# Optimization experiments

Measured on AMD Instinct MI355X. Metric: run time of the kernel, lower is better.

## Reference

```python
import jax, jax.numpy as jnp
import numpy as np

N = 16384; C = 16; H = 256; W = 704
HEADS = 4; PTS = 4; K = 8; DH = C // HEADS
EPS = 1e-3  # BatchNorm eps from module

def _bn(x, g, b):
    # BatchNorm1d in training mode: batch statistics over N
    mu = x.mean(axis=0)
    var = x.var(axis=0)
    return (x - mu) * jax.lax.rsqrt(var + EPS) * g + b

def setup_inputs():
    key = jax.random.key(0)
    ks = jax.random.split(key, 20)
    def w(i, shape, s=0.25):
        return jax.random.normal(ks[i], shape, jnp.float32) * s
    grid_y = jax.random.randint(ks[0], (N,), 0, H)
    grid_x = jax.random.randint(ks[1], (N,), 0, W)
    return {
        "point_features": jax.random.normal(ks[2], (N, C), jnp.float32),
        "image_feat": jax.random.normal(ks[3], (C, H, W), jnp.float32),
        "image_grid": jnp.stack([grid_y, grid_x], axis=1),
        "Wk": w(4, (C, C)), "bk": w(5, (C,)), "gk": jnp.ones((C,)), "betak": jnp.zeros((C,)),
        "Wfc": w(6, (2, C)), "bfc": w(7, (C,)), "gfc": jnp.ones((C,)), "betafc": jnp.zeros((C,)),
        "Wt": w(8, (C, C)), "bt": w(9, (C,)), "gt": jnp.ones((C,)), "betat": jnp.zeros((C,)),
        "Woff": w(10, (C, HEADS * PTS * 2), 0.02), "boff": w(11, (HEADS * PTS * 2,), 0.5),
        "Wattn": w(12, (C, HEADS * PTS), 0.02), "battn": jnp.zeros((HEADS * PTS,)),
        "Wval": w(13, (C, C)), "bval": w(14, (C,)),
        "Wout": w(15, (C, C)), "bout": w(16, (C,)),
        "Wf": w(17, (2 * C, C)), "bf": w(18, (C,)), "gf": jnp.ones((C,)), "betaf": jnp.zeros((C,)),
    }

def _deform_attn(q, image_feat, grid_f, Woff, boff, Wattn, battn, Wval, bval, Wout, bout):
    # MSDeformAttn with 1 level: learned offsets around projected pixel, bilinear sampling
    n = q.shape[0]
    off = (q @ Woff + boff).reshape(n, HEADS, PTS, 2)
    attn = jax.nn.softmax((q @ Wattn + battn).reshape(n, HEADS, PTS), axis=-1)
    val = (image_feat.reshape(C, H * W).T @ Wval + bval).reshape(H * W, HEADS, DH)
    val_h = val.transpose(1, 0, 2)  # [HEADS, HW, DH]
    loc_y = grid_f[:, 0][:, None, None] + off[..., 0]  # [N, HEADS, PTS]
    loc_x = grid_f[:, 1][:, None, None] + off[..., 1]
    y0 = jnp.floor(loc_y); x0 = jnp.floor(loc_x)
    wy = loc_y - y0; wx = loc_x - x0

    def corner(yi, xi, wgt):
        valid = (yi >= 0) & (yi <= H - 1) & (xi >= 0) & (xi <= W - 1)
        yc = jnp.clip(yi, 0, H - 1).astype(jnp.int32)
        xc = jnp.clip(xi, 0, W - 1).astype(jnp.int32)
        idx = (yc * W + xc).transpose(1, 0, 2)  # [HEADS, N, PTS]
        g = jax.vmap(lambda v, i: v[i])(val_h, idx)  # [HEADS, N, PTS, DH]
        return g * (wgt * valid).transpose(1, 0, 2)[..., None]

    samp = (corner(y0, x0, (1 - wy) * (1 - wx))
            + corner(y0, x0 + 1, (1 - wy) * wx)
            + corner(y0 + 1, x0, wy * (1 - wx))
            + corner(y0 + 1, x0 + 1, wy * wx))  # [HEADS, N, PTS, DH]
    out = (samp * attn.transpose(1, 0, 2)[..., None]).sum(axis=2)  # [HEADS, N, DH]
    out = out.transpose(1, 0, 2).reshape(n, C)
    return out @ Wout + bout

def reference(point_features, image_feat, image_grid, Wk, bk, gk, betak, Wfc, bfc, gfc, betafc, Wt, bt, gt, betat, Woff, boff, Wattn, battn, Wval, bval, Wout, bout, Wf, bf, gf, betaf):
    grid_f = image_grid.astype(jnp.float32)
    # KNN over projected pixel coords (cKDTree.query k=K+1, drop self)
    d2 = ((grid_f[:, None, :] - grid_f[None, :, :]) ** 2).sum(-1)
    _, nidx = jax.lax.top_k(-d2, K + 1)
    nidx = nidx[:, 1:]  # [N, K]

    pts = _bn(point_features @ Wk + bk, gk, betak)  # pts_key_proj
    # normalized relative image-plane positions -> fc
    center = grid_f.mean(axis=0)
    rel = grid_f - center
    mx = jnp.abs(rel).max(axis=0)
    mx = jnp.where(mx == 0, 1.0, mx)
    pos = _bn((rel / mx) @ Wfc + bfc, gfc, betafc)

    # gather image feats at projected pixels + KNN-graph neighbor aggregation
    gathered = image_feat[:, image_grid[:, 0], image_grid[:, 1]].T  # [N, C]
    neigh = gathered[nidx].mean(axis=1)  # [N, C]

    q = pts + pos
    img_pre = _deform_attn(q, image_feat, grid_f, Woff, boff, Wattn, battn, Wval, bval, Wout, bout) + neigh

    pts_pre = _bn(pts @ Wt + bt, gt, betat)  # pts_transform
    fuse = jax.nn.relu(jnp.concatenate([pts_pre, img_pre], axis=-1))  # activate_out
    return jax.nn.relu(_bn(fuse @ Wf + bf, gf, betaf))  # fuse_conv
```

## Files before the change

kernel.cpp:

```cpp
#include <hip/hip_runtime.h>
#include <climits>

#define N_ 16384
#define C_ 16
#define H_ 256
#define W_ 704
#define HW_ (H_*W_)
#define NC_ (N_*C_)
#define EPS_ 1e-3f
#define HDR_ 512

typedef unsigned long long ull;


#define GATH_  (HDR_ + 2*NC_)
#define FLIN_  (HDR_ + 8*NC_)
#define VAL_   (HDR_ + 9*NC_)
#define KNNI_  (VAL_ + HW_*16)
#define PARTF_ (KNNI_ + 378256)
#define PS_    (PARTF_ + 8192)
#define GP_    (PS_ + 17408)

#define CAP_ 6144

__device__ __forceinline__ float wsum64(float v){
#pragma unroll
  for (int o = 32; o > 0; o >>= 1) v += __shfl_down(v, o);
  return v;
}

#define LOAD16(dst, src) { const float4* _s=(const float4*)(src); float4 _a=_s[0],_b=_s[1],_c=_s[2],_d=_s[3]; \
  dst[0]=_a.x;dst[1]=_a.y;dst[2]=_a.z;dst[3]=_a.w; dst[4]=_b.x;dst[5]=_b.y;dst[6]=_b.z;dst[7]=_b.w; \
  dst[8]=_c.x;dst[9]=_c.y;dst[10]=_c.z;dst[11]=_c.w; dst[12]=_d.x;dst[13]=_d.y;dst[14]=_d.z;dst[15]=_d.w; }

#define STORE16(dst, src) { float4* _d=(float4*)(dst); \
  _d[0]=make_float4(src[0],src[1],src[2],src[3]); _d[1]=make_float4(src[4],src[5],src[6],src[7]); \
  _d[2]=make_float4(src[8],src[9],src[10],src[11]); _d[3]=make_float4(src[12],src[13],src[14],src[15]); }

__global__ __launch_bounds__(256) void k_init(float* ws){
  if (blockIdx.x < 176){
    int4* c = (int4*)(ws + KNNI_);
    c[blockIdx.x*256 + threadIdx.x] = make_int4(0,0,0,0);
  } else if (threadIdx.x == 0){
    int* ih = (int*)ws;
    ih[2]=INT_MAX; ih[3]=INT_MIN; ih[4]=INT_MAX; ih[5]=INT_MIN;
  }
}

__global__ __launch_bounds__(256) void k_statsprep(
    const float* __restrict__ pf, const float* __restrict__ imf,
    const int* __restrict__ grid,
    const float* __restrict__ Wval, const float* __restrict__ bval,
    float* __restrict__ ws)
{
  int t = threadIdx.x;
  if (blockIdx.x < 64){
    __shared__ float sP[4096];
    __shared__ double sDP[20];
    __shared__ int sh[16];
    int i = blockIdx.x*256 + t;
    { const float4* s4=(const float4*)(pf+i*16);
      float4* d4=(float4*)(sP+t*16);
      d4[0]=s4[0]; d4[1]=s4[1]; d4[2]=s4[2]; d4[3]=s4[3]; }
    int2 g = ((const int2*)grid)[i];
    int* counts = (int*)(ws + KNNI_);
    atomicAdd(&counts[g.x*W_ + g.y], 1);
    int mny=g.x,mxy=g.x,mnx=g.y,mxx=g.y;
#pragma unroll
    for (int o=32;o>0;o>>=1){
      mny=min(mny,__shfl_down(mny,o)); mxy=max(mxy,__shfl_down(mxy,o));
      mnx=min(mnx,__shfl_down(mnx,o)); mxx=max(mxx,__shfl_down(mxx,o));
    }
    int wv = t>>6;
    if ((t&63)==0){ sh[wv]=mny; sh[4+wv]=mxy; sh[8+wv]=mnx; sh[12+wv]=mxx; }
    double yy=(double)g.x, xx=(double)g.y;
    double m0=yy,m1=xx,m2=yy*yy,m3=xx*xx,m4=yy*xx;
#pragma unroll
    for (int o=32;o>0;o>>=1){
      m0+=__shfl_down(m0,o); m1+=__shfl_down(m1,o); m2+=__shfl_down(m2,o);
      m3+=__shfl_down(m3,o); m4+=__shfl_down(m4,o);
    }
    if ((t&63)==0){ sDP[wv*5]=m0; sDP[wv*5+1]=m1; sDP[wv*5+2]=m2; sDP[wv*5+3]=m3; sDP[wv*5+4]=m4; }
    __syncthreads();
    if (t==0){
      int* ih=(int*)ws;
      atomicMin(&ih[2],min(min(sh[0],sh[1]),min(sh[2],sh[3])));
      atomicMax(&ih[3],max(max(sh[4],sh[5]),max(sh[6],sh[7])));
      atomicMin(&ih[4],min(min(sh[8],sh[9]),min(sh[10],sh[11])));
      atomicMax(&ih[5],max(max(sh[12],sh[13]),max(sh[14],sh[15])));
      double* GP=(double*)(ws+GP_)+blockIdx.x*5;
#pragma unroll
      for (int k=0;k<5;++k) GP[k]=sDP[k]+sDP[5+k]+sDP[10+k]+sDP[15+k];
    }
    float* PS = ws + PS_ + blockIdx.x*272;
    int a=t&15, b2=t>>4;
    float acc=0.f;
    for (int i2=0;i2<256;++i2) acc += sP[i2*16+a]*sP[i2*16+b2];
    PS[16+t]=acc;
    if (t<16){
      float s=0.f;
      for (int i2=0;i2<256;++i2) s += sP[i2*16+t];
      PS[t]=s;
    }
  } else if (blockIdx.x < 1088){
    int idx=(blockIdx.x-64)*256+t;
    int i=idx>>4, c=idx&15;
    int2 g=((const int2*)grid)[i];
    ws[GATH_+idx]=imf[c*HW_+g.x*W_+g.y];
  } else {
    __shared__ float sW[256], sb[16];
    sW[t]=Wval[t];
    if (t<16) sb[t]=bval[t];
    __syncthreads();
    int pix=(blockIdx.x-1088)*256+t;
    float a[16];
#pragma unroll
    for (int ci=0;ci<16;++ci) a[ci]=imf[ci*HW_+pix];
    float o[16];
#pragma unroll
    for (int c=0;c<16;++c) o[c]=sb[c];
#pragma unroll
    for (int ci=0;ci<16;++ci){ float v=a[ci];
#pragma unroll
      for (int c=0;c<16;++c) o[c]+=v*sW[ci*16+c];
    }
    STORE16(ws+VAL_+pix*16, o);
  }
}

__global__ __launch_bounds__(256) void k_scanA(float* ws){
  const int* counts = (const int*)(ws + KNNI_);
  int* bsum = (int*)(ws + KNNI_) + 180224 + 180240;
  int t = threadIdx.x;
  int v = counts[blockIdx.x*256 + t];
#pragma unroll
  for (int o=32;o>0;o>>=1) v += __shfl_down(v,o);
  __shared__ int w4[4];
  if ((t&63)==0) w4[t>>6] = v;
  __syncthreads();
  if (t==0) bsum[blockIdx.x] = w4[0]+w4[1]+w4[2]+w4[3];
}

__global__ __launch_bounds__(256) void k_scanB(
    const float* __restrict__ Wk, const float* __restrict__ bk,
    const float* __restrict__ gk, const float* __restrict__ betak,
    const float* __restrict__ Wfc, const float* __restrict__ bfc,
    const float* __restrict__ gfc, const float* __restrict__ betafc,
    const float* __restrict__ Wt, const float* __restrict__ bt,
    const float* __restrict__ gt, const float* __restrict__ betat,
    float* __restrict__ ws)
{
  __shared__ float sS[256], sSum[16];
  __shared__ float skA[16], skC[16];
  __shared__ double sG[5];
  __shared__ float sCtr[4];
  int t = threadIdx.x;
  const float* PS = ws + PS_;
  float acc=0.f, acc2=0.f;
  for (int b=0;b<64;++b){
    acc += PS[b*272 + t];
    if (t<16) acc2 += PS[b*272 + 256 + t];
  }
  if (t<16){ sSum[t]=acc; sS[240+t]=acc2; }
  else sS[t-16]=acc;
  if (t<5){
    const double* GP=(const double*)(ws+GP_);
    double s=0.0;
    for (int b=0;b<64;++b) s += GP[b*5+t];
    sG[t]=s;
  }
  __syncthreads();
  if (t==0){
    const int* ih=(const int*)ws;
    float cy=(float)(sG[0]/(double)N_), cx=(float)(sG[1]/(double)N_);
    float my=fmaxf((float)ih[3]-cy, cy-(float)ih[2]);
    float mx=fmaxf((float)ih[5]-cx, cx-(float)ih[4]);
    if (my==0.f) my=1.f;
    if (mx==0.f) mx=1.f;
    sCtr[0]=cy; sCtr[1]=cx; sCtr[2]=1.f/my; sCtr[3]=1.f/mx;
    ws[264]=cy; ws[265]=cx; ws[266]=sCtr[2]; ws[267]=sCtr[3];
  }
  __syncthreads();
  const float invN = 1.f/(float)N_;
  if (t<16){
    float wc[16];
#pragma unroll
    for (int j=0;j<16;++j) wc[j]=Wk[j*16+t];
    float dotS=0.f;
#pragma unroll
    for (int a2=0;a2<16;++a2) dotS+=sSum[a2]*wc[a2];
    float qd=0.f;
#pragma unroll
    for (int b2=0;b2<16;++b2){
      float inner=0.f;
#pragma unroll
      for (int a2=0;a2<16;++a2) inner+=wc[a2]*sS[b2*16+a2];
      qd+=wc[b2]*inner;
    }
    float bkc=bk[t];
    float mu = dotS*invN + bkc;
    float ex2 = qd*invN + 2.f*bkc*dotS*invN + bkc*bkc;
    float var = ex2 - mu*mu;
    float a = gk[t]/sqrtf(var+EPS_);
    skA[t]=a; skC[t]=betak[t]-mu*a;
    ws[136+t]=a; ws[152+t]=skC[t];
    float cy=sCtr[0], cx=sCtr[1], imy=sCtr[2], imx=sCtr[3];
    float Eyy=((float)(sG[2]/(double)N_) - cy*cy)*imy*imy;
    float Exx=((float)(sG[3]/(double)N_) - cx*cx)*imx*imx;
    float Eyx=((float)(sG[4]/(double)N_) - cy*cx)*imy*imx;
    float W0=Wfc[t], W1=Wfc[16+t];
    float varfc = Eyy*W0*W0 + 2.f*Eyx*W0*W1 + Exx*W1*W1;
    float afc = gfc[t]/sqrtf(varfc+EPS_);
    ws[168+t]=afc; ws[184+t]=betafc[t]-bfc[t]*afc;
  }
  __syncthreads();
  if (t<16){
    float Ac[16];
#pragma unroll
    for (int j=0;j<16;++j){
      float s=0.f;
#pragma unroll
      for (int m=0;m<16;++m) s += Wk[j*16+m]*skA[m]*Wt[m*16+t];
      Ac[j]=s;
    }
    float dc=bt[t];
#pragma unroll
    for (int m=0;m<16;++m) dc += (bk[m]*skA[m]+skC[m])*Wt[m*16+t];
    float dotS=0.f;
#pragma unroll
    for (int a2=0;a2<16;++a2) dotS+=sSum[a2]*Ac[a2];
    float qd=0.f;
#pragma unroll
    for (int b2=0;b2<16;++b2){
      float inner=0.f;
#pragma unroll
      for (int a2=0;a2<16;++a2) inner+=Ac[a2]*sS[b2*16+a2];
      qd+=Ac[b2]*inner;
    }
    float mu = dotS*invN + dc;
    float ex2 = qd*invN + 2.f*dc*dotS*invN + dc*dc;
    float var = ex2 - mu*mu;
    float a = gt[t]/sqrtf(var+EPS_);
    ws[200+t]=a; ws[216+t]=betat[t]-mu*a;
  }
  __syncthreads();
  int* bsum = (int*)(ws + KNNI_) + 180224 + 180240;
  int* boff = bsum + 704;
  __shared__ int sWsum[4];
  __shared__ int sCarry;
  int lane=t&63, wv=t>>6;
  if (t==0) sCarry=0;
  __syncthreads();
  for (int c=0;c<3;++c){
    int idx=c*256+t;
    int v0=(idx<704)?bsum[idx]:0;
    int v=v0;
#pragma unroll
    for (int o=1;o<64;o<<=1){ int xx=__shfl_up(v,o); if (lane>=o) v+=xx; }
    if (lane==63) sWsum[wv]=v;
    __syncthreads();
    int add=sCarry;
    for (int w2=0;w2<wv;++w2) add+=sWsum[w2];
    if (idx<704) boff[idx]=add+v-v0;
    __syncthreads();
    if (t==255) sCarry=add+v;
    __syncthreads();
  }
}

__global__ __launch_bounds__(256) void k_scanC(float* ws){
  int* counts = (int*)(ws + KNNI_);
  int* cellst = counts + 180224;
  const int* boff = counts + 180224 + 180240 + 704;
  __shared__ int sWsum[4];
  int t=threadIdx.x, lane=t&63, wv=t>>6;
  int i=blockIdx.x*256+t;
  int v0=counts[i], v=v0;
#pragma unroll
  for (int o=1;o<64;o<<=1){ int xx=__shfl_up(v,o); if (lane>=o) v+=xx; }
  if (lane==63) sWsum[wv]=v;
  __syncthreads();
  int add=boff[blockIdx.x];
  for (int w2=0;w2<wv;++w2) add+=sWsum[w2];
  int start=add+v-v0;
  cellst[i]=start;
  counts[i]=start;
  if (i==0) cellst[HW_]=N_;
}

__global__ __launch_bounds__(256) void k_scatter(const int* __restrict__ grid, float* __restrict__ ws){
  int i=blockIdx.x*256+threadIdx.x;
  int2 g=((const int2*)grid)[i];
  int* counts=(int*)(ws+KNNI_);
  unsigned* psort=(unsigned*)(counts+180224+180240+704+704);
  int pos=atomicAdd(&counts[g.x*W_+g.y],1);
  psort[pos]=((unsigned)g.x<<24)|((unsigned)g.y<<14)|(unsigned)i;
}

__device__ __forceinline__ void knn_insert(ull* arr, ull key){
  if (key < arr[8]){
    int q=8;
    while (q>0 && arr[q-1]>key){ arr[q]=arr[q-1]; --q; }
    arr[q]=key;
  }
}

__device__ __forceinline__ void scan_rows_global(const int* __restrict__ cellst,
                                                 const unsigned* __restrict__ psort,
                                                 int y, int x, int s,
                                                 int y0, int y1, int x0, int x1, ull* arr){
  for (int yy=y0+s; yy<=y1; yy+=4){
    int rowb=yy*W_;
    int st=cellst[rowb+x0];
    int e =cellst[rowb+x1+1];
    int dy=y-yy, dy2=dy*dy;
    for (int p=st;p<e;++p){
      unsigned u=psort[p];
      int px=(int)((u>>14)&1023);
      int dx=x-px;
      knn_insert(arr, ((ull)(unsigned)(dy2+dx*dx)<<14)|(ull)(u&16383u));
    }
  }
}

__device__ __forceinline__ void scan_rows_band(const unsigned* sBand, const int* sRowBase,
                                               int ya, int y, int x, int s,
                                               int y0, int y1, int x0, int x1, ull* arr){
  for (int yy=y0+s; yy<=y1; yy+=4){
    int j=yy-ya;
    int b=sRowBase[j], e=sRowBase[j+1];
    int lo=b, hi=e;
    while (lo<hi){ int mid=(lo+hi)>>1; int xm=(int)((sBand[mid]>>14)&1023); if (xm<x0) lo=mid+1; else hi=mid; }
    int dy=y-yy, dy2=dy*dy;
    for (int p=lo;p<e;++p){
      unsigned u=sBand[p];
      int px=(int)((u>>14)&1023);
      if (px>x1) break;
      int dx=x-px;
      knn_insert(arr, ((ull)(unsigned)(dy2+dx*dx)<<14)|(ull)(u&16383u));
    }
  }
}

__global__ __launch_bounds__(256) void k_mega(
    const float* __restrict__ pf,
    const float* __restrict__ Wk, const float* __restrict__ bk,
    const float* __restrict__ Wfc, const float* __restrict__ bfc,
    const float* __restrict__ Wt, const float* __restrict__ bt,
    const float* __restrict__ Woff, const float* __restrict__ boff,
    const float* __restrict__ Wattn, const float* __restrict__ battn,
    const float* __restrict__ Wout, const float* __restrict__ bout,
    const float* __restrict__ Wf, const float* __restrict__ bf,
    float* __restrict__ ws)
{
  __shared__ float sWk[256], sWt[256], sWattn[256], sWout[256];
  __shared__ float sWoff[512], sWf[512], sWfc[32];
  __shared__ float sbk[16], sbfc[16], sbt[16], sboff[32], sbattn[16], sbout[16], sbf[16];
  __shared__ float skA[16], skC[16], sfcA[16], sfcC[16], stA[16], stC[16];
  __shared__ float sCtr[4];
  __shared__ unsigned sMe[64];
  __shared__ int sMn, sMx;
  __shared__ unsigned sBand[CAP_];
  __shared__ int sRowBase[80];
  __shared__ float sTl[1024], sNei[1024], sOf[2048], sAt[1024], sSamp[1024], sImg[1024];
  __shared__ float sPart[128];

  const int* cellst = (const int*)(ws+KNNI_)+180224;
  const unsigned* psort = (const unsigned*)((const int*)(ws+KNNI_)+180224+180240+704+704);
  int tid=threadIdx.x, lane=tid&63;
  sWk[tid]=Wk[tid]; sWt[tid]=Wt[tid]; sWattn[tid]=Wattn[tid]; sWout[tid]=Wout[tid];
  sWoff[tid]=Woff[tid]; sWoff[256+tid]=Woff[256+tid];
  sWf[tid]=Wf[tid]; sWf[256+tid]=Wf[256+tid];
  if (tid<32){ sWfc[tid]=Wfc[tid]; sboff[tid]=boff[tid]; }
  if (tid<16){
    sbk[tid]=bk[tid]; sbfc[tid]=bfc[tid]; sbt[tid]=bt[tid]; sbattn[tid]=battn[tid];
    sbout[tid]=bout[tid]; sbf[tid]=bf[tid];
    skA[tid]=ws[136+tid]; skC[tid]=ws[152+tid];
    sfcA[tid]=ws[168+tid]; sfcC[tid]=ws[184+tid];
    stA[tid]=ws[200+tid]; stC[tid]=ws[216+tid];
  }
  if (tid<4) sCtr[tid]=ws[264+tid];
  if (tid==0){ sMn=INT_MAX; sMx=-1; }
  if (tid<64) sMe[tid]=psort[blockIdx.x*64+tid];
  __syncthreads();
  if (tid<64){
    int yy=(int)(sMe[tid]>>24);
    atomicMin(&sMn,yy); atomicMax(&sMx,yy);
  }
  __syncthreads();
  int ya=max(sMn-16,0), yb=min(sMx+16,H_-1);
  int nr=yb-ya+1;
  int p0=cellst[ya*W_], p1=cellst[(yb+1)*W_];
  int count=p1-p0;
  bool fb=(count>CAP_)||(nr>78);
  if (tid<64){
    unsigned me=sMe[tid];
    int i=(int)(me&16383u);
    float yf=(float)(me>>24), xf=(float)((me>>14)&1023u);
    float p[16]; LOAD16(p, pf+i*16);
    float ok[16];
#pragma unroll
    for (int c=0;c<16;++c) ok[c]=sbk[c];
#pragma unroll
    for (int j=0;j<16;++j){ float v=p[j];
#pragma unroll
      for (int c=0;c<16;++c) ok[c]+=v*sWk[j*16+c];
    }
    float ry=(yf-sCtr[0])*sCtr[2], rx=(xf-sCtr[1])*sCtr[3];
    float pts[16], q[16];
#pragma unroll
    for (int c=0;c<16;++c){
      pts[c]=ok[c]*skA[c]+skC[c];
      float pos=ry*sWfc[c]+rx*sWfc[16+c]+sbfc[c];
      q[c]=pts[c]+pos*sfcA[c]+sfcC[c];
    }
    float tv[16];
#pragma unroll
    for (int c=0;c<16;++c) tv[c]=sbt[c];
#pragma unroll
    for (int j=0;j<16;++j){ float v=pts[j];
#pragma unroll
      for (int c=0;c<16;++c) tv[c]+=v*sWt[j*16+c];
    }
#pragma unroll
    for (int c=0;c<16;++c) sTl[tid*16+c]=fmaxf(tv[c]*stA[c]+stC[c],0.f);
    float ov[32];
#pragma unroll
    for (int o=0;o<32;++o) ov[o]=sboff[o];
#pragma unroll
    for (int j=0;j<16;++j){ float v=q[j];
#pragma unroll
      for (int o=0;o<32;++o) ov[o]+=v*sWoff[j*32+o];
    }
#pragma unroll
    for (int o=0;o<32;++o) sOf[tid*32+o]=ov[o];
    float l[16];
#pragma unroll
    for (int c=0;c<16;++c) l[c]=sbattn[c];
#pragma unroll
    for (int j=0;j<16;++j){ float v=q[j];
#pragma unroll
      for (int c=0;c<16;++c) l[c]+=v*sWattn[j*16+c];
    }
#pragma unroll
    for (int h=0;h<4;++h){
      float m=fmaxf(fmaxf(l[h*4],l[h*4+1]),fmaxf(l[h*4+2],l[h*4+3]));
      float e0=expf(l[h*4]-m),e1=expf(l[h*4+1]-m),e2=expf(l[h*4+2]-m),e3=expf(l[h*4+3]-m);
      float inv=1.f/(e0+e1+e2+e3);
      sAt[tid*16+h*4]=e0*inv; sAt[tid*16+h*4+1]=e1*inv;
      sAt[tid*16+h*4+2]=e2*inv; sAt[tid*16+h*4+3]=e3*inv;
    }
  } else {
    int tt=tid-64;
    if (!fb){
      for (int j=tt;j<count;j+=192) sBand[j]=psort[p0+j];
      for (int j=tt;j<=nr;j+=192) sRowBase[j]=cellst[(ya+j)*W_]-p0;
    }
  }
  __syncthreads();
  int s=tid&3, pl=tid>>2;
  unsigned meK=sMe[pl];
  int y=(int)(meK>>24), x=(int)((meK>>14)&1023u);
  int r=8;
  { int y0=max(y-8,0),y1=min(y+8,H_-1),x0=max(x-8,0),x1=min(x+8,W_-1);
    if ((y1-y0+1)*(x1-x0+1)<224) r=16; }
  ull arr[9];
#pragma unroll
  for (int q2=0;q2<9;++q2) arr[q2]=~0ull;
  {
    int y0=max(y-r,0),y1=min(y+r,H_-1),x0=max(x-r,0),x1=min(x+r,W_-1);
    if (!fb) scan_rows_band(sBand,sRowBase,ya,y,x,s,y0,y1,x0,x1,arr);
    else     scan_rows_global(cellst,psort,y,x,s,y0,y1,x0,x1,arr);
  }
  ull m[9];
  bool done=false;
  {
    ull k[9];
#pragma unroll
    for (int q2=0;q2<9;++q2) m[q2]=~0ull;
    int base=lane&~3;
    for (int ss=0;ss<4;++ss){
#pragma unroll
      for (int q2=0;q2<9;++q2) k[q2]=__shfl(arr[q2],base+ss);
      for (int q3=0;q3<9;++q3){
        ull kk=k[q3];
        if (kk>=m[8]) break;
        int q=8; while (q>0&&m[q-1]>kk){ m[q]=m[q-1]; --q; } m[q]=kk;
      }
    }
    int y0=max(y-r,0),y1=min(y+r,H_-1),x0=max(x-r,0),x1=min(x+r,W_-1);
    bool covered=(y0==0)&&(y1==H_-1)&&(x0==0)&&(x1==W_-1);
    bool ok2=covered;
    if (!ok2 && m[8]!=~0ull){ int d9=(int)(m[8]>>14); ok2 = d9 < (r+1)*(r+1); }
    done=ok2;
  }
  while (__ballot(!done)){
    if (!done){
      r<<=1;
      int y0=max(y-r,0),y1=min(y+r,H_-1),x0=max(x-r,0),x1=min(x+r,W_-1);
#pragma unroll
      for (int q2=0;q2<9;++q2) arr[q2]=~0ull;
      if (!fb && r<=16) scan_rows_band(sBand,sRowBase,ya,y,x,s,y0,y1,x0,x1,arr);
      else              scan_rows_global(cellst,psort,y,x,s,y0,y1,x0,x1,arr);
    }
    ull k[9];
    bool doIns=!done;
    if (doIns){
#pragma unroll
      for (int q2=0;q2<9;++q2) m[q2]=~0ull;
    }
    int base=lane&~3;
    for (int ss=0;ss<4;++ss){
#pragma unroll
      for (int q2=0;q2<9;++q2) k[q2]=__shfl(arr[q2],base+ss);
      if (doIns){
        for (int q3=0;q3<9;++q3){
          ull kk=k[q3];
          if (kk>=m[8]) break;
          int q=8; while (q>0&&m[q-1]>kk){ m[q]=m[q-1]; --q; } m[q]=kk;
        }
      }
    }
    if (!done){
      int y0=max(y-r,0),y1=min(y+r,H_-1),x0=max(x-r,0),x1=min(x+r,W_-1);
      bool covered=(y0==0)&&(y1==H_-1)&&(x0==0)&&(x1==W_-1);
      bool ok2=covered;
      if (!ok2 && m[8]!=~0ull){ int d9=(int)(m[8]>>14); ok2 = d9 < (r+1)*(r+1); }
      if (ok2) done=true;
    }
  }
  {
    const float* gath = ws + GATH_;
    float4 acc=make_float4(0.f,0.f,0.f,0.f);
#pragma unroll
    for (int nb=1;nb<9;++nb){
      int idx=(int)(m[nb]&16383ull);
      const float4 g=*(const float4*)(gath+idx*16+s*4);
      acc.x+=g.x; acc.y+=g.y; acc.z+=g.z; acc.w+=g.w;
    }
    ((float4*)sNei)[tid]=make_float4(acc.x*0.125f,acc.y*0.125f,acc.z*0.125f,acc.w*0.125f);
  }
  __syncthreads();
  {
    int p=tid>>2, h=tid&3;
    unsigned meA=sMe[p];
    float yf=(float)(meA>>24), xf=(float)((meA>>14)&1023u);
    const float4* val4=(const float4*)(ws+VAL_);
    float4 acc=make_float4(0.f,0.f,0.f,0.f);
    float offv[8];
#pragma unroll
    for (int o=0;o<8;++o) offv[o]=sOf[p*32+h*8+o];
    float avv[4];
#pragma unroll
    for (int o=0;o<4;++o) avv[o]=sAt[p*16+h*4+o];
#define CORNER(yy,xx,wgt) do{ int _y=(yy),_x=(xx); \
    if ((unsigned)_y<(unsigned)H_ && (unsigned)_x<(unsigned)W_){ \
      float4 _v=val4[(_y*W_+_x)*4+h]; float _w=a*(wgt); \
      acc.x+=_w*_v.x; acc.y+=_w*_v.y; acc.z+=_w*_v.z; acc.w+=_w*_v.w; } }while(0)
#pragma unroll
    for (int pt=0;pt<4;++pt){
      float a=avv[pt];
      float ly=yf+offv[pt*2], lx=xf+offv[pt*2+1];
      float fy=floorf(ly), fx=floorf(lx);
      float wy=ly-fy, wx=lx-fx;
      int y0=(int)fy, x0=(int)fx;
      CORNER(y0,  x0,  (1.f-wy)*(1.f-wx));
      CORNER(y0,  x0+1,(1.f-wy)*wx);
      CORNER(y0+1,x0,  wy*(1.f-wx));
      CORNER(y0+1,x0+1,wy*wx);
    }
#undef CORNER
    ((float4*)sSamp)[tid]=acc;
    __syncthreads();
    float img[4];
#pragma unroll
    for (int k2=0;k2<4;++k2){ int cc=h*4+k2; img[k2]=sbout[cc]+sNei[p*16+cc]; }
#pragma unroll
    for (int j=0;j<16;++j){
      float v=sSamp[p*16+j];
#pragma unroll
      for (int k2=0;k2<4;++k2) img[k2]+=v*sWout[j*16+h*4+k2];
    }
    ((float4*)sImg)[tid]=make_float4(img[0],img[1],img[2],img[3]);
    __syncthreads();
    float fl[4];
#pragma unroll
    for (int k2=0;k2<4;++k2) fl[k2]=sbf[h*4+k2];
#pragma unroll
    for (int j=0;j<16;++j){
      float v1=sTl[p*16+j];
      float v2=fmaxf(sImg[p*16+j],0.f);
#pragma unroll
      for (int k2=0;k2<4;++k2){
        fl[k2]+=v1*sWf[j*16+h*4+k2];
        fl[k2]+=v2*sWf[(16+j)*16+h*4+k2];
      }
    }
    int i3=(int)(meA&16383u);
    ((float4*)(ws+FLIN_+i3*16))[h]=make_float4(fl[0],fl[1],fl[2],fl[3]);
    float s0=fl[0],s1=fl[1],s2=fl[2],s3=fl[3];
    float q0=fl[0]*fl[0],q1=fl[1]*fl[1],q2=fl[2]*fl[2],q3=fl[3]*fl[3];
#pragma unroll
    for (int o=32;o>=4;o>>=1){
      s0+=__shfl_down(s0,o); s1+=__shfl_down(s1,o); s2+=__shfl_down(s2,o); s3+=__shfl_down(s3,o);
      q0+=__shfl_down(q0,o); q1+=__shfl_down(q1,o); q2+=__shfl_down(q2,o); q3+=__shfl_down(q3,o);
    }
    int wave=tid>>6, lane2=tid&63;
    if (lane2<4){
      sPart[wave*32+lane2*4+0]=s0; sPart[wave*32+lane2*4+1]=s1;
      sPart[wave*32+lane2*4+2]=s2; sPart[wave*32+lane2*4+3]=s3;
      sPart[wave*32+16+lane2*4+0]=q0; sPart[wave*32+16+lane2*4+1]=q1;
      sPart[wave*32+16+lane2*4+2]=q2; sPart[wave*32+16+lane2*4+3]=q3;
    }
    __syncthreads();
    if (tid<32){
      float v=sPart[tid]+sPart[32+tid]+sPart[64+tid]+sPart[96+tid];
      (ws+PARTF_)[blockIdx.x*32+tid]=v;
    }
  }
}

__global__ __launch_bounds__(256) void k_outf(const float* __restrict__ gf,
                                              const float* __restrict__ betaf,
                                              const float* __restrict__ ws,
                                              float* __restrict__ out){
  __shared__ float red[256];
  __shared__ float sA[16], sC[16];
  int t=threadIdx.x, slot=t&31, chunk=t>>5;
  const float* part=ws+PARTF_;
  float acc=0.f;
  for (int bb=chunk*32; bb<chunk*32+32; ++bb) acc+=part[bb*32+slot];
  red[t]=acc;
  __syncthreads();
  if (chunk==0){
    float v=red[slot];
#pragma unroll
    for (int k2=1;k2<8;++k2) v+=red[k2*32+slot];
    red[slot]=v;
  }
  __syncthreads();
  if (t<16){
    float mu=red[t]*(1.f/N_);
    float var=red[16+t]*(1.f/N_)-mu*mu;
    float a=gf[t]/sqrtf(var+EPS_);
    sA[t]=a; sC[t]=betaf[t]-mu*a;
  }
  __syncthreads();
  int base=blockIdx.x*4096+t*16;
  float fl[16]; LOAD16(fl, ws+FLIN_+base);
  float o[16];
#pragma unroll
  for (int c=0;c<16;++c) o[c]=fmaxf(fl[c]*sA[c]+sC[c],0.f);
  STORE16(out+base, o);
}

extern "C" void kernel_launch(void* const* d_in, const int* in_sizes, int n_in,
                              void* d_out, int out_size, void* d_ws, size_t ws_size,
                              hipStream_t stream)
{
  const float* pf    = (const float*)d_in[0];
  const float* imf   = (const float*)d_in[1];
  const int*   gridp = (const int*)d_in[2];
  const float* Wk   =(const float*)d_in[3],  *bk   =(const float*)d_in[4];
  const float* gk   =(const float*)d_in[5],  *betak=(const float*)d_in[6];
  const float* Wfc  =(const float*)d_in[7],  *bfc  =(const float*)d_in[8];
  const float* gfc  =(const float*)d_in[9],  *betafc=(const float*)d_in[10];
  const float* Wt   =(const float*)d_in[11], *bt   =(const float*)d_in[12];
  const float* gt   =(const float*)d_in[13], *betat=(const float*)d_in[14];
  const float* Woff =(const float*)d_in[15], *boff =(const float*)d_in[16];
  const float* Wattn=(const float*)d_in[17], *battn=(const float*)d_in[18];
  const float* Wval =(const float*)d_in[19], *bval =(const float*)d_in[20];
  const float* Wout =(const float*)d_in[21], *bout =(const float*)d_in[22];
  const float* Wf   =(const float*)d_in[23], *bf   =(const float*)d_in[24];
  const float* gf   =(const float*)d_in[25], *betaf=(const float*)d_in[26];
  float* ws  = (float*)d_ws;
  float* out = (float*)d_out;

  hipLaunchKernelGGL(k_init,      dim3(177),  dim3(256), 0, stream, ws);
  hipLaunchKernelGGL(k_statsprep, dim3(1792), dim3(256), 0, stream, pf, imf, gridp, Wval, bval, ws);
  hipLaunchKernelGGL(k_scanA,     dim3(704),  dim3(256), 0, stream, ws);
  hipLaunchKernelGGL(k_scanB,     dim3(1),    dim3(256), 0, stream,
                     Wk, bk, gk, betak, Wfc, bfc, gfc, betafc, Wt, bt, gt, betat, ws);
  hipLaunchKernelGGL(k_scanC,     dim3(704),  dim3(256), 0, stream, ws);
  hipLaunchKernelGGL(k_scatter,   dim3(N_/256), dim3(256), 0, stream, gridp, ws);
  hipLaunchKernelGGL(k_mega,      dim3(N_/64), dim3(256), 0, stream,
                     pf, Wk, bk, Wfc, bfc, Wt, bt, Woff, boff, Wattn, battn,
                     Wout, bout, Wf, bf, ws);
  hipLaunchKernelGGL(k_outf,      dim3(64),   dim3(256), 0, stream, gf, betaf, ws, out);
}
```

Before: 224.7 us.

## Halve points per block in k_mega, gather neighbors from transposed image, batch sampling loads

Shrinks the fused k_mega kernel to 32 points per 128-thread block, which doubles the block count and the partial-stat slots consumed by k_outf. It drops the separate per-point gather stage and instead writes a pixel-major transposed copy of the image during the value projection, so neighbor features are read directly by pixel address. Bilinear sampling now computes all clamped addresses and masked weights first and issues the corner loads in batches of eight to raise memory-level parallelism. The trade-offs are an extra full image-sized store in the prep kernel and less work per block over which to amortize the weight loading.

```diff
diff --git a/kernel.cpp b/kernel.cpp
--- a/kernel.cpp
+++ b/kernel.cpp
@@ -12,22 +12,16 @@
 
 typedef unsigned long long ull;
 
-
-#define GATH_  (HDR_ + 2*NC_)
 #define FLIN_  (HDR_ + 8*NC_)
 #define VAL_   (HDR_ + 9*NC_)
 #define KNNI_  (VAL_ + HW_*16)
 #define PARTF_ (KNNI_ + 378256)
-#define PS_    (PARTF_ + 8192)
+#define PS_    (PARTF_ + 16384)
 #define GP_    (PS_ + 17408)
+#define IMFT_  (GP_ + 640)
 
 #define CAP_ 6144
-
-__device__ __forceinline__ float wsum64(float v){
-#pragma unroll
-  for (int o = 32; o > 0; o >>= 1) v += __shfl_down(v, o);
-  return v;
-}
+#define PPB_ 32
 
 #define LOAD16(dst, src) { const float4* _s=(const float4*)(src); float4 _a=_s[0],_b=_s[1],_c=_s[2],_d=_s[3]; \
   dst[0]=_a.x;dst[1]=_a.y;dst[2]=_a.z;dst[3]=_a.w; dst[4]=_b.x;dst[5]=_b.y;dst[6]=_b.z;dst[7]=_b.w; \
@@ -102,20 +96,16 @@
       for (int i2=0;i2<256;++i2) s += sP[i2*16+t];
       PS[t]=s;
     }
-  } else if (blockIdx.x < 1088){
-    int idx=(blockIdx.x-64)*256+t;
-    int i=idx>>4, c=idx&15;
-    int2 g=((const int2*)grid)[i];
-    ws[GATH_+idx]=imf[c*HW_+g.x*W_+g.y];
   } else {
     __shared__ float sW[256], sb[16];
     sW[t]=Wval[t];
     if (t<16) sb[t]=bval[t];
     __syncthreads();
-    int pix=(blockIdx.x-1088)*256+t;
+    int pix=(blockIdx.x-64)*256+t;
     float a[16];
 #pragma unroll
     for (int ci=0;ci<16;++ci) a[ci]=imf[ci*HW_+pix];
+    STORE16(ws+IMFT_+pix*16, a);
     float o[16];
 #pragma unroll
     for (int c=0;c<16;++c) o[c]=sb[c];
@@ -342,8 +332,8 @@
   }
 }
 
-__global__ __launch_bounds__(256) void k_mega(
-    const float* __restrict__ pf,
+__global__ __launch_bounds__(128) void k_mega(
+    const float* __restrict__ pf, const int* __restrict__ grid,
     const float* __restrict__ Wk, const float* __restrict__ bk,
     const float* __restrict__ Wfc, const float* __restrict__ bfc,
     const float* __restrict__ Wt, const float* __restrict__ bt,
@@ -358,19 +348,18 @@
   __shared__ float sbk[16], sbfc[16], sbt[16], sboff[32], sbattn[16], sbout[16], sbf[16];
   __shared__ float skA[16], skC[16], sfcA[16], sfcC[16], stA[16], stC[16];
   __shared__ float sCtr[4];
-  __shared__ unsigned sMe[64];
+  __shared__ unsigned sMe[PPB_];
   __shared__ int sMn, sMx;
   __shared__ unsigned sBand[CAP_];
   __shared__ int sRowBase[80];
-  __shared__ float sTl[1024], sNei[1024], sOf[2048], sAt[1024], sSamp[1024], sImg[1024];
-  __shared__ float sPart[128];
+  __shared__ float sTl[512], sNei[512], sOf[1024], sAt[512], sSamp[512], sImg[512];
+  __shared__ float sPart[64];
 
   const int* cellst = (const int*)(ws+KNNI_)+180224;
   const unsigned* psort = (const unsigned*)((const int*)(ws+KNNI_)+180224+180240+704+704);
   int tid=threadIdx.x, lane=tid&63;
-  sWk[tid]=Wk[tid]; sWt[tid]=Wt[tid]; sWattn[tid]=Wattn[tid]; sWout[tid]=Wout[tid];
-  sWoff[tid]=Woff[tid]; sWoff[256+tid]=Woff[256+tid];
-  sWf[tid]=Wf[tid]; sWf[256+tid]=Wf[256+tid];
+  for (int j=tid;j<256;j+=128){ sWk[j]=Wk[j]; sWt[j]=Wt[j]; sWattn[j]=Wattn[j]; sWout[j]=Wout[j]; }
+  for (int j=tid;j<512;j+=128){ sWoff[j]=Woff[j]; sWf[j]=Wf[j]; }
   if (tid<32){ sWfc[tid]=Wfc[tid]; sboff[tid]=boff[tid]; }
   if (tid<16){
     sbk[tid]=bk[tid]; sbfc[tid]=bfc[tid]; sbt[tid]=bt[tid]; sbattn[tid]=battn[tid];
@@ -381,9 +370,9 @@
   }
   if (tid<4) sCtr[tid]=ws[264+tid];
   if (tid==0){ sMn=INT_MAX; sMx=-1; }
-  if (tid<64) sMe[tid]=psort[blockIdx.x*64+tid];
-  __syncthreads();
-  if (tid<64){
+  if (tid<PPB_) sMe[tid]=psort[blockIdx.x*PPB_+tid];
+  __syncthreads();
+  if (tid<PPB_){
     int yy=(int)(sMe[tid]>>24);
     atomicMin(&sMn,yy); atomicMax(&sMx,yy);
   }
@@ -393,7 +382,7 @@
   int p0=cellst[ya*W_], p1=cellst[(yb+1)*W_];
   int count=p1-p0;
   bool fb=(count>CAP_)||(nr>78);
-  if (tid<64){
+  if (tid<PPB_){
     unsigned me=sMe[tid];
     int i=(int)(me&16383u);
     float yf=(float)(me>>24), xf=(float)((me>>14)&1023u);
@@ -451,10 +440,10 @@
       sAt[tid*16+h*4+2]=e2*inv; sAt[tid*16+h*4+3]=e3*inv;
     }
   } else {
-    int tt=tid-64;
+    int tt=tid-PPB_;
     if (!fb){
-      for (int j=tt;j<count;j+=192) sBand[j]=psort[p0+j];
-      for (int j=tt;j<=nr;j+=192) sRowBase[j]=cellst[(ya+j)*W_]-p0;
+      for (int j=tt;j<count;j+=96) sBand[j]=psort[p0+j];
+      for (int j=tt;j<=nr;j+=96) sRowBase[j]=cellst[(ya+j)*W_]-p0;
     }
   }
   __syncthreads();
@@ -530,13 +519,21 @@
     }
   }
   {
-    const float* gath = ws + GATH_;
+    const float* imfT = ws + IMFT_;
+    int pixn[8];
+#pragma unroll
+    for (int nb=0;nb<8;++nb){
+      int idx=(int)(m[nb+1]&16383ull);
+      int2 g2=((const int2*)grid)[idx];
+      pixn[nb]=g2.x*W_+g2.y;
+    }
+    float4 v[8];
+#pragma unroll
+    for (int nb=0;nb<8;++nb) v[nb]=*(const float4*)(imfT+pixn[nb]*16+s*4);
     float4 acc=make_float4(0.f,0.f,0.f,0.f);
 #pragma unroll
-    for (int nb=1;nb<9;++nb){
-      int idx=(int)(m[nb]&16383ull);
-      const float4 g=*(const float4*)(gath+idx*16+s*4);
-      acc.x+=g.x; acc.y+=g.y; acc.z+=g.z; acc.w+=g.w;
+    for (int nb=0;nb<8;++nb){
+      acc.x+=v[nb].x; acc.y+=v[nb].y; acc.z+=v[nb].z; acc.w+=v[nb].w;
     }
     ((float4*)sNei)[tid]=make_float4(acc.x*0.125f,acc.y*0.125f,acc.z*0.125f,acc.w*0.125f);
   }
@@ -546,30 +543,37 @@
     unsigned meA=sMe[p];
     float yf=(float)(meA>>24), xf=(float)((meA>>14)&1023u);
     const float4* val4=(const float4*)(ws+VAL_);
-    float4 acc=make_float4(0.f,0.f,0.f,0.f);
-    float offv[8];
-#pragma unroll
-    for (int o=0;o<8;++o) offv[o]=sOf[p*32+h*8+o];
-    float avv[4];
-#pragma unroll
-    for (int o=0;o<4;++o) avv[o]=sAt[p*16+h*4+o];
-#define CORNER(yy,xx,wgt) do{ int _y=(yy),_x=(xx); \
-    if ((unsigned)_y<(unsigned)H_ && (unsigned)_x<(unsigned)W_){ \
-      float4 _v=val4[(_y*W_+_x)*4+h]; float _w=a*(wgt); \
-      acc.x+=_w*_v.x; acc.y+=_w*_v.y; acc.z+=_w*_v.z; acc.w+=_w*_v.w; } }while(0)
+    int addr[16];
+    float wgt[16];
 #pragma unroll
     for (int pt=0;pt<4;++pt){
-      float a=avv[pt];
-      float ly=yf+offv[pt*2], lx=xf+offv[pt*2+1];
+      float a=sAt[p*16+h*4+pt];
+      float ly=yf+sOf[p*32+h*8+pt*2], lx=xf+sOf[p*32+h*8+pt*2+1];
       float fy=floorf(ly), fx=floorf(lx);
       float wy=ly-fy, wx=lx-fx;
       int y0=(int)fy, x0=(int)fx;
-      CORNER(y0,  x0,  (1.f-wy)*(1.f-wx));
-      CORNER(y0,  x0+1,(1.f-wy)*wx);
-      CORNER(y0+1,x0,  wy*(1.f-wx));
-      CORNER(y0+1,x0+1,wy*wx);
-    }
-#undef CORNER
+#pragma unroll
+      for (int k2=0;k2<4;++k2){
+        int yy=y0+(k2>>1), xx=x0+(k2&1);
+        bool valid=((unsigned)yy<(unsigned)H_)&&((unsigned)xx<(unsigned)W_);
+        int yc=min(max(yy,0),H_-1), xc=min(max(xx,0),W_-1);
+        addr[pt*4+k2]=(yc*W_+xc)*4+h;
+        float ww=((k2>>1)?wy:(1.f-wy))*((k2&1)?wx:(1.f-wx));
+        wgt[pt*4+k2]=valid?a*ww:0.f;
+      }
+    }
+    float4 acc=make_float4(0.f,0.f,0.f,0.f);
+#pragma unroll
+    for (int b2=0;b2<2;++b2){
+      float4 vv[8];
+#pragma unroll
+      for (int k2=0;k2<8;++k2) vv[k2]=val4[addr[b2*8+k2]];
+#pragma unroll
+      for (int k2=0;k2<8;++k2){
+        float w2=wgt[b2*8+k2];
+        acc.x+=w2*vv[k2].x; acc.y+=w2*vv[k2].y; acc.z+=w2*vv[k2].z; acc.w+=w2*vv[k2].w;
+      }
+    }
     ((float4*)sSamp)[tid]=acc;
     __syncthreads();
     float img[4];
@@ -614,7 +618,7 @@
     }
     __syncthreads();
     if (tid<32){
-      float v=sPart[tid]+sPart[32+tid]+sPart[64+tid]+sPart[96+tid];
+      float v=sPart[tid]+sPart[32+tid];
       (ws+PARTF_)[blockIdx.x*32+tid]=v;
     }
   }
@@ -629,7 +633,7 @@
   int t=threadIdx.x, slot=t&31, chunk=t>>5;
   const float* part=ws+PARTF_;
   float acc=0.f;
-  for (int bb=chunk*32; bb<chunk*32+32; ++bb) acc+=part[bb*32+slot];
+  for (int bb=chunk*64; bb<chunk*64+64; ++bb) acc+=part[bb*32+slot];
   red[t]=acc;
   __syncthreads();
   if (chunk==0){
@@ -676,15 +680,15 @@
   float* ws  = (float*)d_ws;
   float* out = (float*)d_out;
 
-  hipLaunchKernelGGL(k_init,      dim3(177),  dim3(256), 0, stream, ws);
-  hipLaunchKernelGGL(k_statsprep, dim3(1792), dim3(256), 0, stream, pf, imf, gridp, Wval, bval, ws);
-  hipLaunchKernelGGL(k_scanA,     dim3(704),  dim3(256), 0, stream, ws);
-  hipLaunchKernelGGL(k_scanB,     dim3(1),    dim3(256), 0, stream,
+  hipLaunchKernelGGL(k_init,      dim3(177),     dim3(256), 0, stream, ws);
+  hipLaunchKernelGGL(k_statsprep, dim3(768),     dim3(256), 0, stream, pf, imf, gridp, Wval, bval, ws);
+  hipLaunchKernelGGL(k_scanA,     dim3(704),     dim3(256), 0, stream, ws);
+  hipLaunchKernelGGL(k_scanB,     dim3(1),       dim3(256), 0, stream,
                      Wk, bk, gk, betak, Wfc, bfc, gfc, betafc, Wt, bt, gt, betat, ws);
-  hipLaunchKernelGGL(k_scanC,     dim3(704),  dim3(256), 0, stream, ws);
-  hipLaunchKernelGGL(k_scatter,   dim3(N_/256), dim3(256), 0, stream, gridp, ws);
-  hipLaunchKernelGGL(k_mega,      dim3(N_/64), dim3(256), 0, stream,
-                     pf, Wk, bk, Wfc, bfc, Wt, bt, Woff, boff, Wattn, battn,
+  hipLaunchKernelGGL(k_scanC,     dim3(704),     dim3(256), 0, stream, ws);
+  hipLaunchKernelGGL(k_scatter,   dim3(N_/256),  dim3(256), 0, stream, gridp, ws);
+  hipLaunchKernelGGL(k_mega,      dim3(N_/PPB_), dim3(128), 0, stream,
+                     pf, gridp, Wk, bk, Wfc, bfc, Wt, bt, Woff, boff, Wattn, battn,
                      Wout, bout, Wf, bf, ws);
-  hipLaunchKernelGGL(k_outf,      dim3(64),   dim3(256), 0, stream, gf, betaf, ws, out);
-}
+  hipLaunchKernelGGL(k_outf,      dim3(64),      dim3(256), 0, stream, gf, betaf, ws, out);
+}
```

Measured after the change: 234.8 us. 1.04x slower.
